# Optimization experiments

Measured on AMD Instinct MI355X. Metric: run time of the kernel, lower is better.

The kernel has to match this reference:

```python
import jax, jax.numpy as jnp
import numpy as np

BATCH = 2048
INPUT_SIZE = 2048
OUTPUT_SIZE = 2048
N_INPUTS = 6            # fan-in per LUT node
K = 1 << N_INPUTS       # 64 table entries per node


def setup_inputs() -> dict:
    key = jax.random.key(0)
    k1, k2, k3 = jax.random.split(key, 3)
    x = jax.random.uniform(k1, (BATCH, INPUT_SIZE), dtype=jnp.float32)
    table = jax.random.normal(k2, (OUTPUT_SIZE, K), dtype=jnp.float32)
    mapping = jax.random.randint(k3, (OUTPUT_SIZE, N_INPUTS), 0, INPUT_SIZE, dtype=jnp.int64)
    return {"x": x, "table": table, "mapping": mapping}


def reference(x, table, mapping):
    # x: (B, I) in [0,1]; table: (O, 2^n) raw logits; mapping: (O, n) int indices
    O, n = mapping.shape
    Kv = 1 << n
    # per-node input gather -> (B, O, n)
    xg = x[:, mapping]
    # binary codes of the 2^n LUT vertices: bits[k, i] = i-th bit of k
    bits = ((jnp.arange(Kv)[:, None] >> jnp.arange(n)[None, :]) & 1).astype(x.dtype)  # (K, n)
    # vertex probabilities prod_i (x_i if bit else 1-x_i), built by a tiny fixed loop over n
    probs = jnp.ones((x.shape[0], O, Kv), dtype=x.dtype)
    for i in range(n):
        xi = xg[:, :, i][:, :, None]                      # (B, O, 1)
        bi = bits[:, i][None, None, :]                    # (1, 1, K)
        probs = probs * (xi * bi + (1.0 - xi) * (1.0 - bi))
    # differentiable LUT lookup: expected table value under vertex distribution
    out = jnp.einsum('bok,ok->bo', probs, jax.nn.sigmoid(table))  # (B, O)
    return out
```

## Files before the change

kernel.cpp:

```cpp
#include <hip/hip_runtime.h>
#include <math.h>

#define B_TOTAL 2048
#define I_TOTAL 2048
#define O_TOTAL 2048
#define KW 64
#define NIN 6
#define BLOCK 256
#define TILE_B 16
#define CH 4
#define BBLOCKS (B_TOTAL / TILE_B)
#define OBLOCKS (O_TOTAL / BLOCK)

typedef __attribute__((ext_vector_type(2))) float f2;

#define WS_WP  0
#define WS_M32 (32 * O_TOTAL * sizeof(f2))

__global__ void prep_kernel(const float* __restrict__ table,
                            const unsigned int* __restrict__ map_raw,
                            f2* __restrict__ wP,
                            int* __restrict__ m32T)
{
    int idx = blockIdx.x * blockDim.x + threadIdx.x;
    int o = idx >> 5, j = idx & 31;
    float s0 = 1.0f / (1.0f + __expf(-table[o * KW + 2 * j]));
    float s1 = 1.0f / (1.0f + __expf(-table[o * KW + 2 * j + 1]));
    f2 v; v.x = s0; v.y = s1 - s0;
    wP[j * O_TOTAL + o] = v;

    if (idx < O_TOTAL * NIN) {
        bool is64 = ((map_raw[1] | map_raw[3] | map_raw[5] | map_raw[7]) == 0u);
        int val = is64 ? (int)map_raw[2 * idx] : (int)map_raw[idx];
        int oo = idx / NIN, ii = idx - oo * NIN;
        m32T[ii * O_TOTAL + oo] = val;
    }
}

__global__ __launch_bounds__(BLOCK, 4) void lut_main(
    const float* __restrict__ x,
    const f2*    __restrict__ wP,
    const int*   __restrict__ m32T,
    float*       __restrict__ out)
{
    __shared__ float xs[CH * I_TOTAL];

    const int o  = blockIdx.y * BLOCK + threadIdx.x;
    const int b0 = blockIdx.x * TILE_B;

    f2 ww[32];
    #pragma unroll
    for (int j = 0; j < 32; ++j) ww[j] = wP[j * O_TOTAL + o];

    int m[NIN];
    #pragma unroll
    for (int i = 0; i < NIN; ++i) m[i] = m32T[i * O_TOTAL + o];

    for (int c = 0; c < TILE_B / CH; ++c) {
        __syncthreads();
        const float4* src = (const float4*)(x + (size_t)(b0 + c * CH) * I_TOTAL);
        float4* dst = (float4*)xs;
        #pragma unroll
        for (int t = 0; t < (CH * I_TOTAL / 4) / BLOCK; ++t)
            dst[t * BLOCK + threadIdx.x] = src[t * BLOCK + threadIdx.x];
        __syncthreads();

        #pragma unroll
        for (int cr = 0; cr < CH; ++cr) {
            const float* xr = xs + cr * I_TOTAL;
            float xv[NIN];
            #pragma unroll
            for (int i = 0; i < NIN; ++i) xv[i] = xr[m[i]];

            float a5[2];
            #pragma unroll
            for (int h5 = 0; h5 < 2; ++h5) {
                float a4[2];
                #pragma unroll
                for (int h4 = 0; h4 < 2; ++h4) {
                    float a3[2];
                    #pragma unroll
                    for (int h3 = 0; h3 < 2; ++h3) {
                        float a2[2];
                        #pragma unroll
                        for (int h2 = 0; h2 < 2; ++h2) {
                            float a1[2];
                            #pragma unroll
                            for (int h1 = 0; h1 < 2; ++h1) {
                                int j = (((h5 * 2 + h4) * 2 + h3) * 2 + h2) * 2 + h1;
                                f2 w = ww[j];
                                a1[h1] = fmaf(xv[0], w.y, w.x);
                            }
                            a2[h2] = fmaf(xv[1], a1[1] - a1[0], a1[0]);
                        }
                        a3[h3] = fmaf(xv[2], a2[1] - a2[0], a2[0]);
                    }
                    a4[h4] = fmaf(xv[3], a3[1] - a3[0], a3[0]);
                }
                a5[h5] = fmaf(xv[4], a4[1] - a4[0], a4[0]);
            }
            float res = fmaf(xv[5], a5[1] - a5[0], a5[0]);

            out[(size_t)(b0 + c * CH + cr) * O_TOTAL + o] = res;
        }
    }
}

extern "C" void kernel_launch(void* const* d_in, const int* in_sizes, int n_in,
                              void* d_out, int out_size, void* d_ws, size_t ws_size,
                              hipStream_t stream)
{
    const float*        x       = (const float*)d_in[0];
    const float*        table   = (const float*)d_in[1];
    const unsigned int* map_raw = (const unsigned int*)d_in[2];
    float* out  = (float*)d_out;
    f2*    wP   = (f2*) ((char*)d_ws + WS_WP);
    int*   m32T = (int*)((char*)d_ws + WS_M32);

    prep_kernel<<<(O_TOTAL * KW / 2) / BLOCK, BLOCK, 0, stream>>>(table, map_raw, wP, m32T);

    dim3 grid(BBLOCKS, OBLOCKS);
    lut_main<<<grid, dim3(BLOCK), 0, stream>>>(x, wP, m32T, out);
}
```

Measured before the change: 86.04 us.

## Interleave four batch rows in shared memory and evaluate LUT tree with packed f2 math

Shared memory now stores x transposed as float4 per input index, so one LDS.128 gather per mapping index fetches values for four batch rows instead of four scalar gathers. The 6-level lerp tree runs on two-wide float vectors, which lets the compiler emit packed FMA (v_pk_fma_f32) over two batch rows at once. This aims to cut LDS gather instructions and ALU issue count. The staging loop now does strided scalar global loads and builds float4 values, which may coalesce less efficiently than the previous float4 copies.

```diff
diff --git a/kernel.cpp b/kernel.cpp
--- a/kernel.cpp
+++ b/kernel.cpp
@@ -8,11 +8,13 @@
 #define NIN 6
 #define BLOCK 256
 #define TILE_B 16
-#define CH 4
+#define CHB 4
+#define ROUNDS (TILE_B / CHB)
 #define BBLOCKS (B_TOTAL / TILE_B)
 #define OBLOCKS (O_TOTAL / BLOCK)
 
 typedef __attribute__((ext_vector_type(2))) float f2;
+typedef __attribute__((ext_vector_type(4))) float f4;
 
 #define WS_WP  0
 #define WS_M32 (32 * O_TOTAL * sizeof(f2))
@@ -37,13 +39,47 @@
     }
 }
 
+__device__ __forceinline__ f2 bc(float s) { f2 r; r.x = s; r.y = s; return r; }
+
+__device__ __forceinline__ f2 tree6(const f2* __restrict__ ww, const f2 xv[NIN])
+{
+    f2 a5[2];
+    #pragma unroll
+    for (int h5 = 0; h5 < 2; ++h5) {
+        f2 a4[2];
+        #pragma unroll
+        for (int h4 = 0; h4 < 2; ++h4) {
+            f2 a3[2];
+            #pragma unroll
+            for (int h3 = 0; h3 < 2; ++h3) {
+                f2 a2[2];
+                #pragma unroll
+                for (int h2 = 0; h2 < 2; ++h2) {
+                    f2 a1[2];
+                    #pragma unroll
+                    for (int h1 = 0; h1 < 2; ++h1) {
+                        int j = (((h5 * 2 + h4) * 2 + h3) * 2 + h2) * 2 + h1;
+                        f2 w = ww[j];
+                        a1[h1] = __builtin_elementwise_fma(xv[0], bc(w.y), bc(w.x));
+                    }
+                    a2[h2] = __builtin_elementwise_fma(xv[1], a1[1] - a1[0], a1[0]);
+                }
+                a3[h3] = __builtin_elementwise_fma(xv[2], a2[1] - a2[0], a2[0]);
+            }
+            a4[h4] = __builtin_elementwise_fma(xv[3], a3[1] - a3[0], a3[0]);
+        }
+        a5[h5] = __builtin_elementwise_fma(xv[4], a4[1] - a4[0], a4[0]);
+    }
+    return __builtin_elementwise_fma(xv[5], a5[1] - a5[0], a5[0]);
+}
+
 __global__ __launch_bounds__(BLOCK, 4) void lut_main(
     const float* __restrict__ x,
     const f2*    __restrict__ wP,
     const int*   __restrict__ m32T,
     float*       __restrict__ out)
 {
-    __shared__ float xs[CH * I_TOTAL];
+    __shared__ f4 xs[I_TOTAL];
 
     const int o  = blockIdx.y * BLOCK + threadIdx.x;
     const int b0 = blockIdx.x * TILE_B;
@@ -56,53 +92,39 @@
     #pragma unroll
     for (int i = 0; i < NIN; ++i) m[i] = m32T[i * O_TOTAL + o];
 
-    for (int c = 0; c < TILE_B / CH; ++c) {
+    for (int r = 0; r < ROUNDS; ++r) {
         __syncthreads();
-        const float4* src = (const float4*)(x + (size_t)(b0 + c * CH) * I_TOTAL);
-        float4* dst = (float4*)xs;
+        const float* xb = x + (size_t)(b0 + r * CHB) * I_TOTAL;
         #pragma unroll
-        for (int t = 0; t < (CH * I_TOTAL / 4) / BLOCK; ++t)
-            dst[t * BLOCK + threadIdx.x] = src[t * BLOCK + threadIdx.x];
+        for (int t = 0; t < I_TOTAL / BLOCK; ++t) {
+            int idx = t * BLOCK + threadIdx.x;
+            f4 v;
+            v.x = xb[idx];
+            v.y = xb[I_TOTAL + idx];
+            v.z = xb[2 * I_TOTAL + idx];
+            v.w = xb[3 * I_TOTAL + idx];
+            xs[idx] = v;
+        }
         __syncthreads();
 
+        f4 q[NIN];
         #pragma unroll
-        for (int cr = 0; cr < CH; ++cr) {
-            const float* xr = xs + cr * I_TOTAL;
-            float xv[NIN];
-            #pragma unroll
-            for (int i = 0; i < NIN; ++i) xv[i] = xr[m[i]];
+        for (int i = 0; i < NIN; ++i) q[i] = xs[m[i]];
 
-            float a5[2];
-            #pragma unroll
-            for (int h5 = 0; h5 < 2; ++h5) {
-                float a4[2];
-                #pragma unroll
-                for (int h4 = 0; h4 < 2; ++h4) {
-                    float a3[2];
-                    #pragma unroll
-                    for (int h3 = 0; h3 < 2; ++h3) {
-                        float a2[2];
-                        #pragma unroll
-                        for (int h2 = 0; h2 < 2; ++h2) {
-                            float a1[2];
-                            #pragma unroll
-                            for (int h1 = 0; h1 < 2; ++h1) {
-                                int j = (((h5 * 2 + h4) * 2 + h3) * 2 + h2) * 2 + h1;
-                                f2 w = ww[j];
-                                a1[h1] = fmaf(xv[0], w.y, w.x);
-                            }
-                            a2[h2] = fmaf(xv[1], a1[1] - a1[0], a1[0]);
-                        }
-                        a3[h3] = fmaf(xv[2], a2[1] - a2[0], a2[0]);
-                    }
-                    a4[h4] = fmaf(xv[3], a3[1] - a3[0], a3[0]);
-                }
-                a5[h5] = fmaf(xv[4], a4[1] - a4[0], a4[0]);
-            }
-            float res = fmaf(xv[5], a5[1] - a5[0], a5[0]);
+        f2 xlo[NIN], xhi[NIN];
+        #pragma unroll
+        for (int i = 0; i < NIN; ++i) {
+            xlo[i].x = q[i].x; xlo[i].y = q[i].y;
+            xhi[i].x = q[i].z; xhi[i].y = q[i].w;
+        }
+        f2 rlo = tree6(ww, xlo);
+        f2 rhi = tree6(ww, xhi);
 
-            out[(size_t)(b0 + c * CH + cr) * O_TOTAL + o] = res;
-        }
+        float* op = out + (size_t)(b0 + r * CHB) * O_TOTAL + o;
+        op[0 * O_TOTAL] = rlo.x;
+        op[1 * O_TOTAL] = rlo.y;
+        op[2 * O_TOTAL] = rhi.x;
+        op[3 * O_TOTAL] = rhi.y;
     }
 }
 
@@ -117,7 +139,7 @@
     f2*    wP   = (f2*) ((char*)d_ws + WS_WP);
     int*   m32T = (int*)((char*)d_ws + WS_M32);
 
-    prep_kernel<<<(O_TOTAL * KW / 2) / BLOCK, BLOCK, 0, stream>>>(table, map_raw, wP, m32T);
+    prep_kernel<<<(O_TOTAL * 32) / BLOCK, BLOCK, 0, stream>>>(table, map_raw, wP, m32T);
 
     dim3 grid(BBLOCKS, OBLOCKS);
     lut_main<<<grid, dim3(BLOCK), 0, stream>>>(x, wP, m32T, out);
```

Measured after the change: 195.8 us. +127.6%, slower.
